# Performance work log

Measured on AMD Instinct MI355X. Metric: run time of the kernel, lower is better.

The kernel has to match this reference:

```python
import jax, jax.numpy as jnp
import numpy as np

B = 65536
D = 1280   # input_dim (ESM2-650M pooled feature dim)
H = 512    # hidden_dim
T = 4      # number of affinity types (Kd, Ki, IC50, EC50)


def setup_inputs() -> dict:
    key = jax.random.key(0)
    ks = jax.random.split(key, 6)
    features = jax.random.normal(ks[0], (B, D), dtype=jnp.float32)
    affinity_type_idx = jax.random.randint(ks[1], (B,), 0, T, dtype=jnp.int32)
    # Per-type head parameters (stacked over the T heads).
    s1 = 1.0 / np.sqrt(D)
    s2 = 1.0 / np.sqrt(H)
    W1 = jax.random.uniform(ks[2], (T, D, H), jnp.float32, -s1, s1)
    b1 = jax.random.uniform(ks[3], (T, H), jnp.float32, -s1, s1)
    w2 = jax.random.uniform(ks[4], (T, H), jnp.float32, -s2, s2)  # Linear(H,1) weight, squeezed
    b2 = jax.random.uniform(ks[5], (T,), jnp.float32, -s2, s2)
    return {"features": features, "affinity_type_idx": affinity_type_idx,
            "W1": W1, "b1": b1, "w2": w2, "b2": b2}


def reference(features, affinity_type_idx, W1, b1, w2, b2):
    # Compute every head for every sample (T is tiny), then select the routed one.
    # h: (B, T, H)
    h = jnp.einsum('bd,tdh->bth', features, W1) + b1
    h = jax.nn.gelu(h, approximate=False)  # torch nn.GELU default = exact erf GELU
    # preds_all: (B, T) — each head's Linear(H, 1) output, squeezed
    preds_all = jnp.einsum('bth,th->bt', h, w2) + b2
    # Route: pick each sample's own affinity-type head.
    preds = jnp.take_along_axis(preds_all, affinity_type_idx[:, None].astype(jnp.int32), axis=1)
    return preds[:, 0]  # (B,)
```

## Files before the change

### kernel.cpp

```cpp
#include <hip/hip_runtime.h>
#include <math.h>

#define NB 65536
#define ND 1280
#define NH 512
#define NT 4

typedef float f32x4 __attribute__((ext_vector_type(4)));
typedef float f32x2 __attribute__((ext_vector_type(2)));
typedef short s16x8 __attribute__((ext_vector_type(8)));
typedef unsigned int u32x2 __attribute__((ext_vector_type(2)));
typedef unsigned int u32x4 __attribute__((ext_vector_type(4)));
typedef unsigned long long ull;
typedef unsigned short u16;

static __device__ __forceinline__ unsigned f2bf1(float x) {
    union { float f; unsigned u; } v; v.f = x;
    return (v.u + 0x7fffu + ((v.u >> 16) & 1u)) >> 16;
}
static __device__ __forceinline__ unsigned packbf(float a, float b) {
    return f2bf1(a) | (f2bf1(b) << 16);
}
static __device__ __forceinline__ int swz(int a) {
    return a ^ (((a >> 7) & 7) << 4);
}
static __device__ __forceinline__ float gelu_exact(float x) {
    return 0.5f * x * (1.0f + erff(x * 0.70710678118654752f));
}
static __device__ __forceinline__ void gload_lds16(const void* g, void* l) {
    __builtin_amdgcn_global_load_lds(
        (const __attribute__((address_space(1))) unsigned int*)g,
        (__attribute__((address_space(3))) unsigned int*)l, 16, 0, 0);
}

#define SCHEDB __builtin_amdgcn_sched_barrier(0)
#define WAITVM(N) do { asm volatile("s_waitcnt vmcnt(" #N ")" ::: "memory"); SCHEDB; } while (0)
#define WAITLGKM do { asm volatile("s_waitcnt lgkmcnt(0)" ::: "memory"); SCHEDB; } while (0)

__global__ __launch_bounds__(256) void transpose_kernel(const float* __restrict__ W1,
                                                        u16* __restrict__ Wt) {
    __shared__ float tile[64][65];
    int b = blockIdx.x;
    int dt = b % 20; int r = b / 20; int ht = r & 7; int t = r >> 3;
    int d0 = dt * 64, h0 = ht * 64;
    int tid = threadIdx.x;
    const float* src = W1 + ((size_t)t * ND + d0) * NH + h0;
#pragma unroll
    for (int it = 0; it < 16; ++it) {
        int dl = it * 4 + (tid >> 6);
        tile[dl][tid & 63] = src[(size_t)dl * NH + (tid & 63)];
    }
    __syncthreads();
    int hl = tid >> 2, ds = (tid & 3) * 16;
    unsigned pk[8];
#pragma unroll
    for (int j = 0; j < 8; ++j)
        pk[j] = packbf(tile[ds + 2 * j][hl], tile[ds + 2 * j + 1][hl]);
    u16* dst = Wt + ((size_t)(t * NH + h0 + hl)) * ND + d0 + ds;
    *(u32x4*)dst = (u32x4){pk[0], pk[1], pk[2], pk[3]};
    *(u32x4*)(dst + 8) = (u32x4){pk[4], pk[5], pk[6], pk[7]};
}

__global__ __launch_bounds__(256) void count_kernel(const int* __restrict__ idx,
                                                    int* __restrict__ bc) {
    int tid = threadIdx.x;
    int i = blockIdx.x * 256 + tid;
    int t = idx[i];
    int lane = tid & 63, wave = tid >> 6;
    ull b0 = __ballot(t & 1);
    ull b1 = __ballot(t & 2);
    ull mask = ((t & 1) ? b0 : ~b0) & ((t & 2) ? b1 : ~b1);
    int rank = __popcll(mask & ((1ULL << lane) - 1ULL));
    __shared__ int lc[4][4];
    if (tid < 16) ((int*)lc)[tid] = 0;
    __syncthreads();
    if (rank == 0) lc[wave][t] = __popcll(mask);
    __syncthreads();
    if (tid < 4)
        bc[blockIdx.x * 4 + tid] = lc[0][tid] + lc[1][tid] + lc[2][tid] + lc[3][tid];
}

__global__ __launch_bounds__(256) void scan_kernel(const int* __restrict__ bc,
        int* __restrict__ counts, int* __restrict__ base) {
    __shared__ int segtot[64][4];
    __shared__ int segbase[64][4];
    __shared__ int ttot[4];
    int tid = threadIdx.x;
    int t = tid & 3, seg = tid >> 2;
    int s0 = bc[(seg * 4 + 0) * 4 + t];
    int s1 = bc[(seg * 4 + 1) * 4 + t];
    int s2 = bc[(seg * 4 + 2) * 4 + t];
    int s3 = bc[(seg * 4 + 3) * 4 + t];
    segtot[seg][t] = s0 + s1 + s2 + s3;
    __syncthreads();
    if (tid < 4) {
        int run = 0;
        for (int g = 0; g < 64; ++g) { segbase[g][tid] = run; run += segtot[g][tid]; }
        ttot[tid] = run;
        counts[tid] = run;
    }
    __syncthreads();
    int toff = 0;
    for (int u = 0; u < 4; ++u) toff += (u < t) ? ttot[u] : 0;
    int run = toff + segbase[seg][t];
    base[(seg * 4 + 0) * 4 + t] = run; run += s0;
    base[(seg * 4 + 1) * 4 + t] = run; run += s1;
    base[(seg * 4 + 2) * 4 + t] = run; run += s2;
    base[(seg * 4 + 3) * 4 + t] = run;
}

__global__ __launch_bounds__(256) void scatter_kernel(const int* __restrict__ idx,
        const int* __restrict__ base, int* __restrict__ perm,
        const float* __restrict__ b2, float* __restrict__ out) {
    int tid = threadIdx.x;
    int i = blockIdx.x * 256 + tid;
    int t = idx[i];
    int lane = tid & 63, wave = tid >> 6;
    ull b0 = __ballot(t & 1);
    ull b1 = __ballot(t & 2);
    ull mask = ((t & 1) ? b0 : ~b0) & ((t & 2) ? b1 : ~b1);
    int rank = __popcll(mask & ((1ULL << lane) - 1ULL));
    __shared__ int lc[4][4];
    if (tid < 16) ((int*)lc)[tid] = 0;
    __syncthreads();
    if (rank == 0) lc[wave][t] = __popcll(mask);
    __syncthreads();
    int pre = 0;
#pragma unroll
    for (int w = 0; w < 4; ++w) pre += (w < wave) ? lc[w][t] : 0;
    perm[base[blockIdx.x * 4 + t] + pre + rank] = i;
    out[i] = b2[t];
}

__global__ __launch_bounds__(256, 2) void gemm_pipe(
        const float* __restrict__ feat, const u16* __restrict__ Wt,
        const float* __restrict__ b1, const float* __restrict__ w2,
        const int* __restrict__ perm, const int* __restrict__ counts,
        float* __restrict__ partials, float* __restrict__ out, int use_partials) {
    __shared__ char smem[65536];

    int bx = blockIdx.x;
    int r8 = bx & 7, m8 = bx >> 3;
    int ct = m8 & 3, q = m8 >> 2;
    int g = q * 8 + r8;
    int t = g >> 9, tile_m = g & 511;
    int cnt = counts[t];
    int tilebase = tile_m * 128;
    if (tilebase >= cnt) return;
    int off_t = 0;
    for (int u = 0; u < t; ++u) off_t += counts[u];

    int tid = threadIdx.x;
    int lane = tid & 63, wave = tid >> 6;
    int wr = wave >> 1, wc = wave & 1;
    int hc0 = ct * 128;

    unsigned aoff[8];
#pragma unroll
    for (int i = 0; i < 8; ++i) {
        int r = tilebase + i * 16 + (tid >> 4);
        if (r > cnt - 1) r = cnt - 1;
        aoff[i] = (unsigned)perm[off_t + r] * ND + (tid & 15) * 4;
    }
    unsigned boff[4];
#pragma unroll
    for (int j = 0; j < 4; ++j) {
        int a = wave * 4096 + j * 1024 + lane * 16;
        int col = a >> 7, chunk = (a >> 4) & 7;
        boff[j] = (unsigned)((t * NH + hc0 + col) * ND + ((chunk ^ (col & 7)) * 8));
    }

    f32x4 acc[4][4];
#pragma unroll
    for (int a = 0; a < 4; ++a)
#pragma unroll
        for (int b = 0; b < 4; ++b) acc[a][b] = (f32x4){0.f, 0.f, 0.f, 0.f};

    f32x4 apf0[8], apf1[8];

    auto LOADA = [&](f32x4 (&arr)[8], int kt) {
#pragma unroll
        for (int i = 0; i < 8; ++i)
            arr[i] = *(const f32x4*)(feat + aoff[i] + kt * 64);
    };
    auto STAGE_B = [&](int kt, int buf) {
        char* dst = smem + 32768 + buf * 16384 + wave * 4096;
#pragma unroll
        for (int j = 0; j < 4; ++j)
            gload_lds16(Wt + boff[j] + kt * 64, dst + j * 1024);
    };
    auto WRITEA = [&](const f32x4 (&arr)[8], int buf) {
        char* ab = smem + buf * 16384;
#pragma unroll
        for (int i = 0; i < 8; ++i) {
            int row = i * 16 + (tid >> 4);
            u32x2 v;
            v.x = packbf(arr[i][0], arr[i][1]);
            v.y = packbf(arr[i][2], arr[i][3]);
            *(u32x2*)(ab + swz(row * 128 + (tid & 15) * 8)) = v;
        }
    };
    auto COMPUTE = [&](int buf) {
        char* ab = smem + buf * 16384;
        char* bb = smem + 32768 + buf * 16384;
#pragma unroll
        for (int ks = 0; ks < 2; ++ks) {
            int kbyte = ks * 64 + (lane >> 4) * 16;
            s16x8 af[4], bf[4];
#pragma unroll
            for (int f = 0; f < 4; ++f) {
                int rowA = wr * 64 + f * 16 + (lane & 15);
                af[f] = *(const s16x8*)(ab + swz(rowA * 128 + kbyte));
                int colB = wc * 64 + f * 16 + (lane & 15);
                bf[f] = *(const s16x8*)(bb + swz(colB * 128 + kbyte));
            }
#pragma unroll
            for (int fm = 0; fm < 4; ++fm)
#pragma unroll
                for (int fn = 0; fn < 4; ++fn)
                    acc[fm][fn] = __builtin_amdgcn_mfma_f32_16x16x32_bf16(
                        af[fm], bf[fn], acc[fm][fn], 0, 0, 0);
        }
    };

    STAGE_B(0, 0);
    SCHEDB;
    LOADA(apf0, 0);
    SCHEDB;
    LOADA(apf1, 1);
    SCHEDB;
    WAITVM(8);
    WRITEA(apf0, 0);
    WAITLGKM;
    __builtin_amdgcn_s_barrier();

#pragma unroll 1
    for (int kt = 0; kt < 18; kt += 2) {
        STAGE_B(kt + 1, 1);
        SCHEDB;
        LOADA(apf0, kt + 2);
        SCHEDB;
        COMPUTE(0);
        WAITVM(12);
        WRITEA(apf1, 1);
        WAITVM(8);
        WAITLGKM;
        __builtin_amdgcn_s_barrier();
        STAGE_B(kt + 2, 0);
        SCHEDB;
        LOADA(apf1, kt + 3);
        SCHEDB;
        COMPUTE(1);
        WAITVM(12);
        WRITEA(apf0, 0);
        WAITVM(8);
        WAITLGKM;
        __builtin_amdgcn_s_barrier();
    }

    STAGE_B(19, 1);
    SCHEDB;
    COMPUTE(0);
    WAITVM(4);
    WRITEA(apf1, 1);
    WAITVM(0);
    WAITLGKM;
    __builtin_amdgcn_s_barrier();
    COMPUTE(1);

    float part[4][4];
#pragma unroll
    for (int fm = 0; fm < 4; ++fm)
#pragma unroll
        for (int r = 0; r < 4; ++r) part[fm][r] = 0.f;
#pragma unroll
    for (int fn = 0; fn < 4; ++fn) {
        int h = hc0 + wc * 64 + fn * 16 + (lane & 15);
        float b1v = b1[t * NH + h];
        float w2v = w2[t * NH + h];
#pragma unroll
        for (int fm = 0; fm < 4; ++fm)
#pragma unroll
            for (int r = 0; r < 4; ++r) {
                float v = acc[fm][fn][r] + b1v;
                part[fm][r] += gelu_exact(v) * w2v;
            }
    }
#pragma unroll
    for (int m = 1; m <= 8; m <<= 1)
#pragma unroll
        for (int fm = 0; fm < 4; ++fm)
#pragma unroll
            for (int r = 0; r < 4; ++r)
                part[fm][r] += __shfl_xor(part[fm][r], m, 64);

    if ((lane & 15) == 0) {
        int slot = ct * 2 + wc;
#pragma unroll
        for (int fm = 0; fm < 4; ++fm)
#pragma unroll
            for (int r = 0; r < 4; ++r) {
                int row = wr * 64 + fm * 16 + (lane >> 4) * 4 + r;
                int gr = tilebase + row;
                if (gr < cnt) {
                    int s = perm[off_t + gr];
                    if (use_partials)
                        partials[(size_t)s * 8 + slot] = part[fm][r];
                    else
                        atomicAdd(&out[s], part[fm][r]);
                }
            }
    }
}

__global__ __launch_bounds__(256, 2) void gemm_fallback(
        const float* __restrict__ feat, const float* __restrict__ W1,
        const float* __restrict__ b1, const float* __restrict__ w2,
        const int* __restrict__ perm, const int* __restrict__ counts,
        float* __restrict__ partials, float* __restrict__ out, int use_partials) {
    __shared__ char smem[32768];
    int bx = blockIdx.x;
    int r8 = bx & 7, m8 = bx >> 3;
    int ct = m8 & 3, q = m8 >> 2;
    int g = q * 8 + r8;
    int t = g >> 9, tile_m = g & 511;
    int cnt = counts[t];
    int tilebase = tile_m * 128;
    if (tilebase >= cnt) return;
    int off_t = 0;
    for (int u = 0; u < t; ++u) off_t += counts[u];

    int tid = threadIdx.x;
    int lane = tid & 63, wave = tid >> 6;
    int wr = wave >> 1, wc = wave & 1;
    int hc0 = ct * 128;

    unsigned aoff[8];
#pragma unroll
    for (int i = 0; i < 8; ++i) {
        int r = tilebase + i * 16 + (tid >> 4);
        if (r > cnt - 1) r = cnt - 1;
        int s = perm[off_t + r];
        aoff[i] = (unsigned)s * ND + (tid & 15) * 4;
    }
    f32x4 acc[4][4];
#pragma unroll
    for (int a = 0; a < 4; ++a)
#pragma unroll
        for (int b = 0; b < 4; ++b) acc[a][b] = (f32x4){0.f, 0.f, 0.f, 0.f};
    f32x4 apf[8];
    int cpair = (tid & 63) * 2;
    int kkbase = tid >> 6;
    const float* wbase = W1 + (size_t)t * ND * NH + hc0 + cpair;
    f32x2 bpf[4][4];
    auto LOADA = [&](int k0) {
#pragma unroll
        for (int i = 0; i < 8; ++i)
            apf[i] = *(const f32x4*)(feat + aoff[i] + k0);
    };
    auto LOADB = [&](int k0) {
#pragma unroll
        for (int qq = 0; qq < 4; ++qq) {
            int d = k0 + (kkbase + qq * 4) * 4;
#pragma unroll
            for (int e = 0; e < 4; ++e)
                bpf[qq][e] = *(const f32x2*)(wbase + (size_t)(d + e) * NH);
        }
    };
    auto WRITEA = [&]() {
#pragma unroll
        for (int i = 0; i < 8; ++i) {
            int row = i * 16 + (tid >> 4);
            u32x2 v;
            v.x = packbf(apf[i][0], apf[i][1]);
            v.y = packbf(apf[i][2], apf[i][3]);
            *(u32x2*)(smem + swz(row * 128 + (tid & 15) * 8)) = v;
        }
    };
    auto WRITEB = [&]() {
#pragma unroll
        for (int qq = 0; qq < 4; ++qq) {
            int kk = kkbase + qq * 4;
#pragma unroll
            for (int j = 0; j < 2; ++j) {
                u32x2 v;
                v.x = packbf(bpf[qq][0][j], bpf[qq][1][j]);
                v.y = packbf(bpf[qq][2][j], bpf[qq][3][j]);
                *(u32x2*)(smem + 16384 + swz((cpair + j) * 128 + kk * 8)) = v;
            }
        }
    };
    auto COMPUTE_KS = [&](int ks) {
        int kbyte = ks * 64 + (lane >> 4) * 16;
        s16x8 af[4], bf[4];
#pragma unroll
        for (int f = 0; f < 4; ++f) {
            int rowA = wr * 64 + f * 16 + (lane & 15);
            af[f] = *(const s16x8*)(smem + swz(rowA * 128 + kbyte));
            int colB = wc * 64 + f * 16 + (lane & 15);
            bf[f] = *(const s16x8*)(smem + 16384 + swz(colB * 128 + kbyte));
        }
#pragma unroll
        for (int fm = 0; fm < 4; ++fm)
#pragma unroll
            for (int fn = 0; fn < 4; ++fn)
                acc[fm][fn] = __builtin_amdgcn_mfma_f32_16x16x32_bf16(
                    af[fm], bf[fn], acc[fm][fn], 0, 0, 0);
    };
    LOADA(0); LOADB(0);
    WRITEA(); WRITEB();
    __syncthreads();
#pragma unroll 1
    for (int kt = 0; kt < 20; ++kt) {
        bool nxt = (kt + 1 < 20);
        if (nxt) LOADA((kt + 1) * 64);
        COMPUTE_KS(0);
        if (nxt) LOADB((kt + 1) * 64);
        COMPUTE_KS(1);
        if (nxt) {
            __syncthreads();
            WRITEA(); WRITEB();
            __syncthreads();
        }
    }
    float part[4][4];
#pragma unroll
    for (int fm = 0; fm < 4; ++fm)
#pragma unroll
        for (int r = 0; r < 4; ++r) part[fm][r] = 0.f;
#pragma unroll
    for (int fn = 0; fn < 4; ++fn) {
        int h = hc0 + wc * 64 + fn * 16 + (lane & 15);
        float b1v = b1[t * NH + h];
        float w2v = w2[t * NH + h];
#pragma unroll
        for (int fm = 0; fm < 4; ++fm)
#pragma unroll
            for (int r = 0; r < 4; ++r) {
                float v = acc[fm][fn][r] + b1v;
                part[fm][r] += gelu_exact(v) * w2v;
            }
    }
#pragma unroll
    for (int m = 1; m <= 8; m <<= 1)
#pragma unroll
        for (int fm = 0; fm < 4; ++fm)
#pragma unroll
            for (int r = 0; r < 4; ++r)
                part[fm][r] += __shfl_xor(part[fm][r], m, 64);
    if ((lane & 15) == 0) {
        int slot = ct * 2 + wc;
#pragma unroll
        for (int fm = 0; fm < 4; ++fm)
#pragma unroll
            for (int r = 0; r < 4; ++r) {
                int row = wr * 64 + fm * 16 + (lane >> 4) * 4 + r;
                int gr = tilebase + row;
                if (gr < cnt) {
                    int s = perm[off_t + gr];
                    if (use_partials)
                        partials[(size_t)s * 8 + slot] = part[fm][r];
                    else
                        atomicAdd(&out[s], part[fm][r]);
                }
            }
    }
}

__global__ __launch_bounds__(256) void reduce_kernel(const float* __restrict__ partials,
        const int* __restrict__ idx, const float* __restrict__ b2,
        float* __restrict__ out) {
    int i = blockIdx.x * 256 + threadIdx.x;
    const float* p = partials + (size_t)i * 8;
    float s = b2[idx[i]];
#pragma unroll
    for (int j = 0; j < 8; ++j) s += p[j];
    out[i] = s;
}

extern "C" void kernel_launch(void* const* d_in, const int* in_sizes, int n_in,
                              void* d_out, int out_size, void* d_ws, size_t ws_size,
                              hipStream_t stream) {
    (void)in_sizes; (void)n_in; (void)out_size;
    const float* feat = (const float*)d_in[0];
    const int*   idx  = (const int*)d_in[1];
    const float* W1   = (const float*)d_in[2];
    const float* b1   = (const float*)d_in[3];
    const float* w2   = (const float*)d_in[4];
    const float* b2   = (const float*)d_in[5];
    float* out = (float*)d_out;

    char* ws = (char*)d_ws;
    int* counts  = (int*)ws;
    int* bc      = (int*)(ws + 64);
    int* base    = (int*)(ws + 64 + 4096);
    int* perm    = (int*)(ws + 64 + 8192);
    float* partials = (float*)(ws + 64 + 8192 + (size_t)NB * 4);
    u16* Wt = (u16*)(ws + 64 + 8192 + (size_t)NB * 4 + (size_t)NB * 32);
    size_t need_part = 64 + 8192 + (size_t)NB * 4 + (size_t)NB * 32;
    size_t need_full = need_part + (size_t)NT * ND * NH * 2;
    int use_partials = (ws_size >= need_part) ? 1 : 0;
    int use_wt = (ws_size >= need_full) ? 1 : 0;

    if (use_wt)
        transpose_kernel<<<NT * 8 * 20, 256, 0, stream>>>(W1, Wt);
    count_kernel<<<NB / 256, 256, 0, stream>>>(idx, bc);
    scan_kernel<<<1, 256, 0, stream>>>(bc, counts, base);
    scatter_kernel<<<NB / 256, 256, 0, stream>>>(idx, base, perm, b2, out);
    if (use_wt)
        gemm_pipe<<<8192, 256, 0, stream>>>(feat, Wt, b1, w2, perm, counts,
                                            partials, out, use_partials);
    else
        gemm_fallback<<<8192, 256, 0, stream>>>(feat, W1, b1, w2, perm, counts,
                                                partials, out, use_partials);
    if (use_partials)
        reduce_kernel<<<NB / 256, 256, 0, stream>>>(partials, idx, b2, out);
}
```

Before: 221.9 us.

## Stage fp32 features directly to LDS and compact the tile grid

The GEMM now loads fp32 feature rows straight into LDS with global_load_lds, applying an XOR swizzle, instead of staging them through registers. The bf16 conversion moves to after the LDS read, just before the MFMAs. The K tile shrinks to 32 and LDS drops to 48KB so three blocks can fit per CU. A tmap prefix of per-type tile counts lets the launch use a compact grid of 2080 blocks instead of 8192 mostly-empty blocks. This removes register-staged A loads and early-exit block overhead, but doubles the number of barriers per K and moves the conversion work into the compute loop.

After: 231.7 us. 1.04x slower.

```diff
diff --git a/kernel.cpp b/kernel.cpp
--- a/kernel.cpp
+++ b/kernel.cpp
@@ -21,6 +21,9 @@
 static __device__ __forceinline__ unsigned packbf(float a, float b) {
     return f2bf1(a) | (f2bf1(b) << 16);
 }
+static __device__ __forceinline__ s16x8 as_s16x8(u32x4 v) {
+    union { u32x4 u; s16x8 s; } x; x.u = v; return x.s;
+}
 static __device__ __forceinline__ int swz(int a) {
     return a ^ (((a >> 7) & 7) << 4);
 }
@@ -35,7 +38,6 @@
 
 #define SCHEDB __builtin_amdgcn_sched_barrier(0)
 #define WAITVM(N) do { asm volatile("s_waitcnt vmcnt(" #N ")" ::: "memory"); SCHEDB; } while (0)
-#define WAITLGKM do { asm volatile("s_waitcnt lgkmcnt(0)" ::: "memory"); SCHEDB; } while (0)
 
 __global__ __launch_bounds__(256) void transpose_kernel(const float* __restrict__ W1,
                                                         u16* __restrict__ Wt) {
@@ -81,7 +83,7 @@
 }
 
 __global__ __launch_bounds__(256) void scan_kernel(const int* __restrict__ bc,
-        int* __restrict__ counts, int* __restrict__ base) {
+        int* __restrict__ counts, int* __restrict__ base, int* __restrict__ tmap) {
     __shared__ int segtot[64][4];
     __shared__ int segbase[64][4];
     __shared__ int ttot[4];
@@ -100,6 +102,11 @@
         counts[tid] = run;
     }
     __syncthreads();
+    if (tid == 0) {
+        int s = 0;
+        tmap[0] = 0;
+        for (int u = 0; u < 4; ++u) { s += (ttot[u] + 127) >> 7; tmap[u + 1] = s; }
+    }
     int toff = 0;
     for (int u = 0; u < 4; ++u) toff += (u < t) ? ttot[u] : 0;
     int run = toff + segbase[seg][t];
@@ -132,43 +139,65 @@
     out[i] = b2[t];
 }
 
-__global__ __launch_bounds__(256, 2) void gemm_pipe(
+__global__ __launch_bounds__(256, 3) void gemm_glds(
         const float* __restrict__ feat, const u16* __restrict__ Wt,
         const float* __restrict__ b1, const float* __restrict__ w2,
         const int* __restrict__ perm, const int* __restrict__ counts,
+        const int* __restrict__ tmap,
         float* __restrict__ partials, float* __restrict__ out, int use_partials) {
-    __shared__ char smem[65536];
+    __shared__ char smem[49152];
 
     int bx = blockIdx.x;
     int r8 = bx & 7, m8 = bx >> 3;
     int ct = m8 & 3, q = m8 >> 2;
-    int g = q * 8 + r8;
-    int t = g >> 9, tile_m = g & 511;
+    int tau = q * 8 + r8;
+    if (tau >= tmap[4]) return;
+    int t = 0;
+#pragma unroll
+    for (int u = 0; u < 3; ++u) t += (tau >= tmap[u + 1]) ? 1 : 0;
+    int tile_m = tau - tmap[t];
     int cnt = counts[t];
     int tilebase = tile_m * 128;
-    if (tilebase >= cnt) return;
     int off_t = 0;
     for (int u = 0; u < t; ++u) off_t += counts[u];
 
     int tid = threadIdx.x;
     int lane = tid & 63, wave = tid >> 6;
     int wr = wave >> 1, wc = wave & 1;
+    int rl = lane & 15, q0 = lane >> 4;
     int hc0 = ct * 128;
 
-    unsigned aoff[8];
-#pragma unroll
-    for (int i = 0; i < 8; ++i) {
-        int r = tilebase + i * 16 + (tid >> 4);
+    unsigned asrc[4];
+    unsigned axor = (unsigned)(((tid & 7) ^ ((tid >> 3) & 7)) * 4);
+#pragma unroll
+    for (int p = 0; p < 4; ++p) {
+        int r = tilebase + p * 32 + (tid >> 3);
         if (r > cnt - 1) r = cnt - 1;
-        aoff[i] = (unsigned)perm[off_t + r] * ND + (tid & 15) * 4;
-    }
-    unsigned boff[4];
-#pragma unroll
-    for (int j = 0; j < 4; ++j) {
-        int a = wave * 4096 + j * 1024 + lane * 16;
-        int col = a >> 7, chunk = (a >> 4) & 7;
-        boff[j] = (unsigned)((t * NH + hc0 + col) * ND + ((chunk ^ (col & 7)) * 8));
-    }
+        asrc[p] = (unsigned)perm[off_t + r] * ND + axor;
+    }
+    unsigned bsrc[2];
+    unsigned bxor = (unsigned)(((tid & 3) ^ ((tid >> 3) & 3)) * 8);
+#pragma unroll
+    for (int p = 0; p < 2; ++p) {
+        int col = p * 64 + (tid >> 2);
+        bsrc[p] = (unsigned)(t * NH + hc0 + col) * ND + bxor;
+    }
+    int ldsw = wave * 1024;
+
+    auto STAGE = [&](int kt, int c) {
+        char* ab = smem + c * 16384;
+        char* bb = smem + 32768 + c * 8192;
+#pragma unroll
+        for (int p = 0; p < 4; ++p)
+            gload_lds16(feat + asrc[p] + kt * 32, ab + p * 4096 + ldsw);
+#pragma unroll
+        for (int p = 0; p < 2; ++p)
+            gload_lds16(Wt + bsrc[p] + kt * 32, bb + p * 4096 + ldsw);
+    };
+
+    int ar0 = (wr * 64 + rl) * 128 + (((q0 * 2)     ^ (rl & 7)) << 4);
+    int ar1 = (wr * 64 + rl) * 128 + (((q0 * 2 + 1) ^ (rl & 7)) << 4);
+    int br0 = (wc * 64 + rl) * 64  + ((q0 ^ ((rl >> 1) & 3)) << 4);
 
     f32x4 acc[4][4];
 #pragma unroll
@@ -176,97 +205,62 @@
 #pragma unroll
         for (int b = 0; b < 4; ++b) acc[a][b] = (f32x4){0.f, 0.f, 0.f, 0.f};
 
-    f32x4 apf0[8], apf1[8];
-
-    auto LOADA = [&](f32x4 (&arr)[8], int kt) {
-#pragma unroll
-        for (int i = 0; i < 8; ++i)
-            arr[i] = *(const f32x4*)(feat + aoff[i] + kt * 64);
-    };
-    auto STAGE_B = [&](int kt, int buf) {
-        char* dst = smem + 32768 + buf * 16384 + wave * 4096;
-#pragma unroll
-        for (int j = 0; j < 4; ++j)
-            gload_lds16(Wt + boff[j] + kt * 64, dst + j * 1024);
-    };
-    auto WRITEA = [&](const f32x4 (&arr)[8], int buf) {
-        char* ab = smem + buf * 16384;
-#pragma unroll
-        for (int i = 0; i < 8; ++i) {
-            int row = i * 16 + (tid >> 4);
-            u32x2 v;
-            v.x = packbf(arr[i][0], arr[i][1]);
-            v.y = packbf(arr[i][2], arr[i][3]);
-            *(u32x2*)(ab + swz(row * 128 + (tid & 15) * 8)) = v;
+    auto COMPUTE = [&](int c) {
+        char* ab = smem + c * 16384;
+        char* bb = smem + 32768 + c * 8192;
+        f32x4 a0[4], a1[4];
+        s16x8 bf[4];
+#pragma unroll
+        for (int f = 0; f < 4; ++f) {
+            a0[f] = *(const f32x4*)(ab + f * 2048 + ar0);
+            a1[f] = *(const f32x4*)(ab + f * 2048 + ar1);
+            bf[f] = *(const s16x8*)(bb + f * 1024 + br0);
         }
-    };
-    auto COMPUTE = [&](int buf) {
-        char* ab = smem + buf * 16384;
-        char* bb = smem + 32768 + buf * 16384;
-#pragma unroll
-        for (int ks = 0; ks < 2; ++ks) {
-            int kbyte = ks * 64 + (lane >> 4) * 16;
-            s16x8 af[4], bf[4];
-#pragma unroll
-            for (int f = 0; f < 4; ++f) {
-                int rowA = wr * 64 + f * 16 + (lane & 15);
-                af[f] = *(const s16x8*)(ab + swz(rowA * 128 + kbyte));
-                int colB = wc * 64 + f * 16 + (lane & 15);
-                bf[f] = *(const s16x8*)(bb + swz(colB * 128 + kbyte));
-            }
-#pragma unroll
-            for (int fm = 0; fm < 4; ++fm)
-#pragma unroll
-                for (int fn = 0; fn < 4; ++fn)
-                    acc[fm][fn] = __builtin_amdgcn_mfma_f32_16x16x32_bf16(
-                        af[fm], bf[fn], acc[fm][fn], 0, 0, 0);
-        }
-    };
-
-    STAGE_B(0, 0);
-    SCHEDB;
-    LOADA(apf0, 0);
-    SCHEDB;
-    LOADA(apf1, 1);
-    SCHEDB;
-    WAITVM(8);
-    WRITEA(apf0, 0);
-    WAITLGKM;
+        u32x4 abf[4];
+#pragma unroll
+        for (int f = 0; f < 4; ++f)
+            abf[f] = (u32x4){packbf(a0[f][0], a0[f][1]), packbf(a0[f][2], a0[f][3]),
+                             packbf(a1[f][0], a1[f][1]), packbf(a1[f][2], a1[f][3])};
+#pragma unroll
+        for (int fm = 0; fm < 4; ++fm)
+#pragma unroll
+            for (int fn = 0; fn < 4; ++fn)
+                acc[fm][fn] = __builtin_amdgcn_mfma_f32_16x16x32_bf16(
+                    as_s16x8(abf[fm]), bf[fn], acc[fm][fn], 0, 0, 0);
+    };
+
+    STAGE(0, 0); SCHEDB;
+    STAGE(1, 1); SCHEDB;
+
+#pragma unroll 1
+    for (int kt = 0; kt < 36; kt += 2) {
+        WAITVM(6);
+        __builtin_amdgcn_s_barrier();
+        COMPUTE(0);
+        __builtin_amdgcn_s_barrier();
+        STAGE(kt + 2, 0); SCHEDB;
+        WAITVM(6);
+        __builtin_amdgcn_s_barrier();
+        COMPUTE(1);
+        __builtin_amdgcn_s_barrier();
+        STAGE(kt + 3, 1); SCHEDB;
+    }
+    WAITVM(6);
     __builtin_amdgcn_s_barrier();
-
-#pragma unroll 1
-    for (int kt = 0; kt < 18; kt += 2) {
-        STAGE_B(kt + 1, 1);
-        SCHEDB;
-        LOADA(apf0, kt + 2);
-        SCHEDB;
-        COMPUTE(0);
-        WAITVM(12);
-        WRITEA(apf1, 1);
-        WAITVM(8);
-        WAITLGKM;
-        __builtin_amdgcn_s_barrier();
-        STAGE_B(kt + 2, 0);
-        SCHEDB;
-        LOADA(apf1, kt + 3);
-        SCHEDB;
-        COMPUTE(1);
-        WAITVM(12);
-        WRITEA(apf0, 0);
-        WAITVM(8);
-        WAITLGKM;
-        __builtin_amdgcn_s_barrier();
-    }
-
-    STAGE_B(19, 1);
-    SCHEDB;
     COMPUTE(0);
-    WAITVM(4);
-    WRITEA(apf1, 1);
-    WAITVM(0);
-    WAITLGKM;
+    __builtin_amdgcn_s_barrier();
+    STAGE(38, 0); SCHEDB;
+    WAITVM(6);
     __builtin_amdgcn_s_barrier();
     COMPUTE(1);
+    __builtin_amdgcn_s_barrier();
+    STAGE(39, 1); SCHEDB;
+    WAITVM(6);
+    __builtin_amdgcn_s_barrier();
+    COMPUTE(0);
+    WAITVM(0);
+    __builtin_amdgcn_s_barrier();
+    COMPUTE(1);
 
     float part[4][4];
 #pragma unroll
@@ -275,7 +269,7 @@
         for (int r = 0; r < 4; ++r) part[fm][r] = 0.f;
 #pragma unroll
     for (int fn = 0; fn < 4; ++fn) {
-        int h = hc0 + wc * 64 + fn * 16 + (lane & 15);
+        int h = hc0 + wc * 64 + fn * 16 + rl;
         float b1v = b1[t * NH + h];
         float w2v = w2[t * NH + h];
 #pragma unroll
@@ -294,13 +288,13 @@
             for (int r = 0; r < 4; ++r)
                 part[fm][r] += __shfl_xor(part[fm][r], m, 64);
 
-    if ((lane & 15) == 0) {
+    if (rl == 0) {
         int slot = ct * 2 + wc;
 #pragma unroll
         for (int fm = 0; fm < 4; ++fm)
 #pragma unroll
             for (int r = 0; r < 4; ++r) {
-                int row = wr * 64 + fm * 16 + (lane >> 4) * 4 + r;
+                int row = wr * 64 + fm * 16 + q0 * 4 + r;
                 int gr = tilebase + row;
                 if (gr < cnt) {
                     int s = perm[off_t + gr];
@@ -494,10 +488,11 @@
     int* counts  = (int*)ws;
     int* bc      = (int*)(ws + 64);
     int* base    = (int*)(ws + 64 + 4096);
-    int* perm    = (int*)(ws + 64 + 8192);
-    float* partials = (float*)(ws + 64 + 8192 + (size_t)NB * 4);
-    u16* Wt = (u16*)(ws + 64 + 8192 + (size_t)NB * 4 + (size_t)NB * 32);
-    size_t need_part = 64 + 8192 + (size_t)NB * 4 + (size_t)NB * 32;
+    int* tmap    = (int*)(ws + 64 + 8192);
+    int* perm    = (int*)(ws + 128 + 8192);
+    float* partials = (float*)(ws + 128 + 8192 + (size_t)NB * 4);
+    u16* Wt = (u16*)(ws + 128 + 8192 + (size_t)NB * 4 + (size_t)NB * 32);
+    size_t need_part = 128 + 8192 + (size_t)NB * 4 + (size_t)NB * 32;
     size_t need_full = need_part + (size_t)NT * ND * NH * 2;
     int use_partials = (ws_size >= need_part) ? 1 : 0;
     int use_wt = (ws_size >= need_full) ? 1 : 0;
@@ -505,10 +500,10 @@
     if (use_wt)
         transpose_kernel<<<NT * 8 * 20, 256, 0, stream>>>(W1, Wt);
     count_kernel<<<NB / 256, 256, 0, stream>>>(idx, bc);
-    scan_kernel<<<1, 256, 0, stream>>>(bc, counts, base);
+    scan_kernel<<<1, 256, 0, stream>>>(bc, counts, base, tmap);
     scatter_kernel<<<NB / 256, 256, 0, stream>>>(idx, base, perm, b2, out);
     if (use_wt)
-        gemm_pipe<<<8192, 256, 0, stream>>>(feat, Wt, b1, w2, perm, counts,
+        gemm_glds<<<2080, 256, 0, stream>>>(feat, Wt, b1, w2, perm, counts, tmap,
                                             partials, out, use_partials);
     else
         gemm_fallback<<<8192, 256, 0, stream>>>(feat, W1, b1, w2, perm, counts,
```

## Replace double-buffered GEMM pipeline with single-buffer loop and compact tile map

Applied to the files above, without the earlier changes.

The grouped GEMM drops its hand-scheduled double-buffered LDS pipeline (explicit waitcnt and sched barriers) for a single 32KB buffer with plain __syncthreads, and raises launch bounds to 4 blocks per CU. The scan kernel now emits a prefix map of per-type tile counts, so the GEMM grid is sized to the real number of tiles (2080 blocks) instead of launching 8192 and early-exiting most of them. The intent is higher occupancy and less launch waste, at the cost of less overlap between global loads, LDS writes and MFMA compute within each block.

New measurement: 877.8 us. 296% more time.

```diff
diff --git a/kernel.cpp b/kernel.cpp
--- a/kernel.cpp
+++ b/kernel.cpp
@@ -32,10 +32,6 @@
         (const __attribute__((address_space(1))) unsigned int*)g,
         (__attribute__((address_space(3))) unsigned int*)l, 16, 0, 0);
 }
-
-#define SCHEDB __builtin_amdgcn_sched_barrier(0)
-#define WAITVM(N) do { asm volatile("s_waitcnt vmcnt(" #N ")" ::: "memory"); SCHEDB; } while (0)
-#define WAITLGKM do { asm volatile("s_waitcnt lgkmcnt(0)" ::: "memory"); SCHEDB; } while (0)
 
 __global__ __launch_bounds__(256) void transpose_kernel(const float* __restrict__ W1,
                                                         u16* __restrict__ Wt) {
@@ -81,7 +77,7 @@
 }
 
 __global__ __launch_bounds__(256) void scan_kernel(const int* __restrict__ bc,
-        int* __restrict__ counts, int* __restrict__ base) {
+        int* __restrict__ counts, int* __restrict__ base, int* __restrict__ tmap) {
     __shared__ int segtot[64][4];
     __shared__ int segbase[64][4];
     __shared__ int ttot[4];
@@ -100,6 +96,11 @@
         counts[tid] = run;
     }
     __syncthreads();
+    if (tid == 0) {
+        int s = 0;
+        tmap[0] = 0;
+        for (int u = 0; u < 4; ++u) { s += (ttot[u] + 127) >> 7; tmap[u + 1] = s; }
+    }
     int toff = 0;
     for (int u = 0; u < 4; ++u) toff += (u < t) ? ttot[u] : 0;
     int run = toff + segbase[seg][t];
@@ -132,21 +133,25 @@
     out[i] = b2[t];
 }
 
-__global__ __launch_bounds__(256, 2) void gemm_pipe(
+__global__ __launch_bounds__(256, 4) void gemm_kernel(
         const float* __restrict__ feat, const u16* __restrict__ Wt,
         const float* __restrict__ b1, const float* __restrict__ w2,
         const int* __restrict__ perm, const int* __restrict__ counts,
+        const int* __restrict__ tmap,
         float* __restrict__ partials, float* __restrict__ out, int use_partials) {
-    __shared__ char smem[65536];
+    __shared__ char smem[32768];
 
     int bx = blockIdx.x;
     int r8 = bx & 7, m8 = bx >> 3;
-    int ct = m8 & 3, q = m8 >> 2;
-    int g = q * 8 + r8;
-    int t = g >> 9, tile_m = g & 511;
+    int ct = m8 & 3;
+    int tau = (m8 >> 2) * 8 + r8;
+    if (tau >= tmap[4]) return;
+    int t = 0;
+#pragma unroll
+    for (int u = 0; u < 3; ++u) t += (tau >= tmap[u + 1]) ? 1 : 0;
+    int tile_m = tau - tmap[t];
     int cnt = counts[t];
     int tilebase = tile_m * 128;
-    if (tilebase >= cnt) return;
     int off_t = 0;
     for (int u = 0; u < t; ++u) off_t += counts[u];
 
@@ -162,6 +167,48 @@
         if (r > cnt - 1) r = cnt - 1;
         aoff[i] = (unsigned)perm[off_t + r] * ND + (tid & 15) * 4;
     }
+
+    f32x4 acc[4][4];
+#pragma unroll
+    for (int a = 0; a < 4; ++a)
+#pragma unroll
+        for (int b = 0; b < 4; ++b) acc[a][b] = (f32x4){0.f, 0.f, 0.f, 0.f};
+
+    f32x4 apf[8];
+
+    auto LOADA = [&](int k0) {
+#pragma unroll
+        for (int i = 0; i < 8; ++i)
+            apf[i] = *(const f32x4*)(feat + aoff[i] + k0);
+    };
+    auto WRITEA = [&]() {
+#pragma unroll
+        for (int i = 0; i < 8; ++i) {
+            int row = i * 16 + (tid >> 4);
+            u32x2 v;
+            v.x = packbf(apf[i][0], apf[i][1]);
+            v.y = packbf(apf[i][2], apf[i][3]);
+            *(u32x2*)(smem + swz(row * 128 + (tid & 15) * 8)) = v;
+        }
+    };
+    auto COMPUTE_KS = [&](int ks) {
+        int kbyte = ks * 64 + (lane >> 4) * 16;
+        s16x8 af[4], bf[4];
+#pragma unroll
+        for (int f = 0; f < 4; ++f) {
+            int rowA = wr * 64 + f * 16 + (lane & 15);
+            af[f] = *(const s16x8*)(smem + swz(rowA * 128 + kbyte));
+            int colB = wc * 64 + f * 16 + (lane & 15);
+            bf[f] = *(const s16x8*)(smem + 16384 + swz(colB * 128 + kbyte));
+        }
+#pragma unroll
+        for (int fm = 0; fm < 4; ++fm)
+#pragma unroll
+            for (int fn = 0; fn < 4; ++fn)
+                acc[fm][fn] = __builtin_amdgcn_mfma_f32_16x16x32_bf16(
+                    af[fm], bf[fn], acc[fm][fn], 0, 0, 0);
+    };
+
     unsigned boff[4];
 #pragma unroll
     for (int j = 0; j < 4; ++j) {
@@ -169,104 +216,29 @@
         int col = a >> 7, chunk = (a >> 4) & 7;
         boff[j] = (unsigned)((t * NH + hc0 + col) * ND + ((chunk ^ (col & 7)) * 8));
     }
-
-    f32x4 acc[4][4];
-#pragma unroll
-    for (int a = 0; a < 4; ++a)
-#pragma unroll
-        for (int b = 0; b < 4; ++b) acc[a][b] = (f32x4){0.f, 0.f, 0.f, 0.f};
-
-    f32x4 apf0[8], apf1[8];
-
-    auto LOADA = [&](f32x4 (&arr)[8], int kt) {
-#pragma unroll
-        for (int i = 0; i < 8; ++i)
-            arr[i] = *(const f32x4*)(feat + aoff[i] + kt * 64);
-    };
-    auto STAGE_B = [&](int kt, int buf) {
-        char* dst = smem + 32768 + buf * 16384 + wave * 4096;
+    auto STAGE_B = [&](int kt) {
 #pragma unroll
         for (int j = 0; j < 4; ++j)
-            gload_lds16(Wt + boff[j] + kt * 64, dst + j * 1024);
-    };
-    auto WRITEA = [&](const f32x4 (&arr)[8], int buf) {
-        char* ab = smem + buf * 16384;
-#pragma unroll
-        for (int i = 0; i < 8; ++i) {
-            int row = i * 16 + (tid >> 4);
-            u32x2 v;
-            v.x = packbf(arr[i][0], arr[i][1]);
-            v.y = packbf(arr[i][2], arr[i][3]);
-            *(u32x2*)(ab + swz(row * 128 + (tid & 15) * 8)) = v;
-        }
-    };
-    auto COMPUTE = [&](int buf) {
-        char* ab = smem + buf * 16384;
-        char* bb = smem + 32768 + buf * 16384;
-#pragma unroll
-        for (int ks = 0; ks < 2; ++ks) {
-            int kbyte = ks * 64 + (lane >> 4) * 16;
-            s16x8 af[4], bf[4];
-#pragma unroll
-            for (int f = 0; f < 4; ++f) {
-                int rowA = wr * 64 + f * 16 + (lane & 15);
-                af[f] = *(const s16x8*)(ab + swz(rowA * 128 + kbyte));
-                int colB = wc * 64 + f * 16 + (lane & 15);
-                bf[f] = *(const s16x8*)(bb + swz(colB * 128 + kbyte));
-            }
-#pragma unroll
-            for (int fm = 0; fm < 4; ++fm)
-#pragma unroll
-                for (int fn = 0; fn < 4; ++fn)
-                    acc[fm][fn] = __builtin_amdgcn_mfma_f32_16x16x32_bf16(
-                        af[fm], bf[fn], acc[fm][fn], 0, 0, 0);
-        }
-    };
-
-    STAGE_B(0, 0);
-    SCHEDB;
-    LOADA(apf0, 0);
-    SCHEDB;
-    LOADA(apf1, 1);
-    SCHEDB;
-    WAITVM(8);
-    WRITEA(apf0, 0);
-    WAITLGKM;
-    __builtin_amdgcn_s_barrier();
-
+            gload_lds16(Wt + boff[j] + kt * 64,
+                        smem + 16384 + wave * 4096 + j * 1024);
+    };
+
+    LOADA(0);
+    STAGE_B(0);
+    WRITEA();
+    __syncthreads();
 #pragma unroll 1
-    for (int kt = 0; kt < 18; kt += 2) {
-        STAGE_B(kt + 1, 1);
-        SCHEDB;
-        LOADA(apf0, kt + 2);
-        SCHEDB;
-        COMPUTE(0);
-        WAITVM(12);
-        WRITEA(apf1, 1);
-        WAITVM(8);
-        WAITLGKM;
-        __builtin_amdgcn_s_barrier();
-        STAGE_B(kt + 2, 0);
-        SCHEDB;
-        LOADA(apf1, kt + 3);
-        SCHEDB;
-        COMPUTE(1);
-        WAITVM(12);
-        WRITEA(apf0, 0);
-        WAITVM(8);
-        WAITLGKM;
-        __builtin_amdgcn_s_barrier();
-    }
-
-    STAGE_B(19, 1);
-    SCHEDB;
-    COMPUTE(0);
-    WAITVM(4);
-    WRITEA(apf1, 1);
-    WAITVM(0);
-    WAITLGKM;
-    __builtin_amdgcn_s_barrier();
-    COMPUTE(1);
+    for (int kt = 0; kt < 20; ++kt) {
+        if (kt < 19) LOADA((kt + 1) * 64);
+        COMPUTE_KS(0);
+        COMPUTE_KS(1);
+        __syncthreads();
+        if (kt < 19) {
+            STAGE_B(kt + 1);
+            WRITEA();
+            __syncthreads();
+        }
+    }
 
     float part[4][4];
 #pragma unroll
@@ -494,10 +466,11 @@
     int* counts  = (int*)ws;
     int* bc      = (int*)(ws + 64);
     int* base    = (int*)(ws + 64 + 4096);
-    int* perm    = (int*)(ws + 64 + 8192);
-    float* partials = (float*)(ws + 64 + 8192 + (size_t)NB * 4);
-    u16* Wt = (u16*)(ws + 64 + 8192 + (size_t)NB * 4 + (size_t)NB * 32);
-    size_t need_part = 64 + 8192 + (size_t)NB * 4 + (size_t)NB * 32;
+    int* tmap    = (int*)(ws + 64 + 8192);
+    int* perm    = (int*)(ws + 128 + 8192);
+    float* partials = (float*)(ws + 128 + 8192 + (size_t)NB * 4);
+    u16* Wt = (u16*)(ws + 128 + 8192 + (size_t)NB * 4 + (size_t)NB * 32);
+    size_t need_part = 128 + 8192 + (size_t)NB * 4 + (size_t)NB * 32;
     size_t need_full = need_part + (size_t)NT * ND * NH * 2;
     int use_partials = (ws_size >= need_part) ? 1 : 0;
     int use_wt = (ws_size >= need_full) ? 1 : 0;
@@ -505,11 +478,11 @@
     if (use_wt)
         transpose_kernel<<<NT * 8 * 20, 256, 0, stream>>>(W1, Wt);
     count_kernel<<<NB / 256, 256, 0, stream>>>(idx, bc);
-    scan_kernel<<<1, 256, 0, stream>>>(bc, counts, base);
+    scan_kernel<<<1, 256, 0, stream>>>(bc, counts, base, tmap);
     scatter_kernel<<<NB / 256, 256, 0, stream>>>(idx, base, perm, b2, out);
     if (use_wt)
-        gemm_pipe<<<8192, 256, 0, stream>>>(feat, Wt, b1, w2, perm, counts,
-                                            partials, out, use_partials);
+        gemm_kernel<<<2080, 256, 0, stream>>>(feat, Wt, b1, w2, perm, counts, tmap,
+                                              partials, out, use_partials);
     else
         gemm_fallback<<<8192, 256, 0, stream>>>(feat, W1, b1, w2, perm, counts,
                                                 partials, out, use_partials);
```
